# Performance work log

Measured on AMD Instinct MI355X. Metric: run time of the kernel, lower is better.

Reference implementation:

```python
import jax, jax.numpy as jnp
import numpy as np

B, S, D = 4, 4096, 256  # batch, seq_len, input_dims == num_hiddens
NEG = -1e9

def setup_inputs() -> dict:
    key = jax.random.key(0)
    ks = jax.random.split(key, 9)
    sd = 1.0 / np.sqrt(D)
    x = jax.random.normal(ks[0], (B, S, D), dtype=jnp.float32)
    mask = jnp.tril(jnp.ones((S, S), dtype=jnp.int32))[None, :, :]  # [1,S,S] causal
    # Linear params: y = x @ W.T + b (torch convention); store as [in,out] for einsum
    wq = jax.random.uniform(ks[1], (D, D), jnp.float32, -sd, sd)
    bq = jax.random.uniform(ks[2], (D,), jnp.float32, -sd, sd)
    wk = jax.random.uniform(ks[3], (D, D), jnp.float32, -sd, sd)
    bk = jax.random.uniform(ks[4], (D,), jnp.float32, -sd, sd)
    wv = jax.random.uniform(ks[5], (D, D), jnp.float32, -sd, sd)
    bv = jax.random.uniform(ks[6], (D,), jnp.float32, -sd, sd)
    wo = jax.random.uniform(ks[7], (D, D), jnp.float32, -sd, sd)
    bo = jax.random.uniform(ks[8], (D,), jnp.float32, -sd, sd)
    return {"x": x, "mask": mask, "wq": wq, "bq": bq, "wk": wk, "bk": bk,
            "wv": wv, "bv": bv, "wo": wo, "bo": bo}

def reference(x, mask, wq, bq, wk, bk, wv, bv, wo, bo):
    # Single-head scaled dot-product self-attention (dropout = identity / eval mode)
    q = jnp.einsum('bsd,df->bsf', x, wq) + bq
    k = jnp.einsum('bsd,df->bsf', x, wk) + bk
    v = jnp.einsum('bsd,df->bsf', x, wv) + bv
    attn = jnp.einsum('bqf,bkf->bqk', q, k) / jnp.sqrt(jnp.float32(q.shape[-1]))
    attn = jnp.where(mask == 0, NEG, attn)  # masked_fill(mask==0, -1e9)
    attn = jax.nn.softmax(attn, axis=-1)
    score = jnp.einsum('bqk,bkf->bqf', attn, v)
    out = jnp.einsum('bsf,fd->bsd', score, wo) + bo
    return out
```

## Files before the change

kernel.cpp:

```cpp
#include <hip/hip_runtime.h>
#include <stdint.h>
#include <type_traits>

typedef __attribute__((ext_vector_type(8))) short short8;
typedef __attribute__((ext_vector_type(4))) short s16x4;
typedef __attribute__((ext_vector_type(4))) float f32x4;

#define S_LEN 4096
#define D_DIM 256
#define BATCH 4

__device__ __forceinline__ f32x4 mfma16(short8 a, short8 b, f32x4 c) {
    return __builtin_amdgcn_mfma_f32_16x16x32_bf16(a, b, c, 0, 0, 0);
}

__device__ __forceinline__ short f2bf(float x) {
    uint32_t u = __float_as_uint(x);
    uint32_t r = (u + 0x7FFFu + ((u >> 16) & 1u)) >> 16;
    return (short)r;
}
__device__ __forceinline__ float bf2f(short s) {
    uint32_t u = ((uint32_t)(uint16_t)s) << 16;
    return __uint_as_float(u);
}

__device__ __forceinline__ void gload16(const short* g, short* l) {
    __builtin_amdgcn_global_load_lds(
        (const __attribute__((address_space(1))) void*)g,
        (__attribute__((address_space(3))) void*)l, 16, 0, 0);
}

__global__ __launch_bounds__(256) void xbf_conv(
    const float* __restrict__ x, short* __restrict__ xb)
{
    int i = blockIdx.x * 256 + threadIdx.x;
    f32x4 a = *reinterpret_cast<const f32x4*>(x + (size_t)i * 8);
    f32x4 b = *reinterpret_cast<const f32x4*>(x + (size_t)i * 8 + 4);
    short8 r;
#pragma unroll
    for (int k = 0; k < 4; ++k) r[k] = f2bf(a[k]);
#pragma unroll
    for (int k = 0; k < 4; ++k) r[k + 4] = f2bf(b[k]);
    *reinterpret_cast<short8*>(xb + (size_t)i * 8) = r;
}

__global__ __launch_bounds__(256) void transpose_w(
    const float* __restrict__ wq, const float* __restrict__ wk,
    const float* __restrict__ wv, const float* __restrict__ wo,
    short* __restrict__ out)
{
    __shared__ float t[16][17];
    const float* in = blockIdx.z == 0 ? wq : blockIdx.z == 1 ? wk
                    : blockIdx.z == 2 ? wv : wo;
    short* o = out + (size_t)blockIdx.z * 65536;
    const int x0 = blockIdx.x * 16, y0 = blockIdx.y * 16;
    const int tx = threadIdx.x, ty = threadIdx.y;
    t[ty][tx] = in[(y0 + ty) * 256 + x0 + tx];
    __syncthreads();
    o[(size_t)(x0 + ty) * 256 + y0 + tx] = f2bf(t[tx][ty]);
}

__global__ __launch_bounds__(256) void gemm_qkv(
    const short* __restrict__ A, const short* __restrict__ Bt,
    const float* __restrict__ bq, const float* __restrict__ bk,
    const float* __restrict__ bv,
    short* __restrict__ QF, short* __restrict__ KF, short* __restrict__ VF)
{
    __shared__ short As[128 * 64];
    __shared__ short Bs[128 * 64];
    const int tid = threadIdx.x;
    const int lane = tid & 63;
    const int w = tid >> 6;
    const int wr = w >> 1, wc = w & 1;
    const int lo = lane & 15, hi = lane >> 4;
    const size_t m0 = (size_t)blockIdx.y * 128, n0 = (size_t)blockIdx.x * 128;
    const int reg = (int)(n0 >> 8);
    const float* bias = reg == 0 ? bq : (reg == 1 ? bk : bv);

    f32x4 acc[4][4] = {};

    for (int kt = 0; kt < 4; ++kt) {
#pragma unroll
        for (int i = 0; i < 4; ++i) {
            int c = i * 4 + w;
            int s = c * 64 + lane;
            int row = s >> 3, ke = (s & 7) * 8;
            gload16(A  + (m0 + row) * 256 + kt * 64 + ke, As + c * 512);
            gload16(Bt + (n0 + row) * 256 + kt * 64 + ke, Bs + c * 512);
        }
        __syncthreads();
#pragma unroll
        for (int kk = 0; kk < 2; ++kk) {
            short8 af[4], bf[4];
#pragma unroll
            for (int m = 0; m < 4; ++m)
                af[m] = *reinterpret_cast<const short8*>(&As[(wr * 64 + m * 16 + lo) * 64 + kk * 32 + hi * 8]);
#pragma unroll
            for (int n = 0; n < 4; ++n)
                bf[n] = *reinterpret_cast<const short8*>(&Bs[(wc * 64 + n * 16 + lo) * 64 + kk * 32 + hi * 8]);
#pragma unroll
            for (int m = 0; m < 4; ++m)
#pragma unroll
                for (int n = 0; n < 4; ++n)
                    acc[m][n] = mfma16(af[m], bf[n], acc[m][n]);
        }
        __syncthreads();
    }

#pragma unroll
    for (int m = 0; m < 4; ++m) {
#pragma unroll
        for (int n = 0; n < 4; ++n) {
#pragma unroll
            for (int j = 0; j < 4; ++j) {
                size_t row = m0 + wr * 64 + m * 16 + hi * 4 + j;
                int f = (int)((n0 + wc * 64 + n * 16 + lo) & 255);
                float v = acc[m][n][j] + bias[f];
                int b = (int)(row >> 12), R = (int)(row & 4095);
                if (reg == 0) {
                    int jt = R >> 4, lk = R & 15;
                    int kk = f >> 5, q = f & 31, hk = q >> 3, e = q & 7;
                    QF[((((size_t)(b * 256 + jt) * 8 + kk) * 64) + hk * 16 + lk) * 8 + e] = f2bf(v);
                } else if (reg == 1) {
                    int ktile = R >> 6, nn = (R >> 4) & 3, lk = R & 15;
                    int kk = f >> 5, q = f & 31, hk = q >> 3, e = q & 7;
                    KF[(((((size_t)(b * 64 + ktile) * 8 + kk) * 4 + nn) * 64) + hk * 16 + lk) * 8 + e] = f2bf(v);
                } else {
                    int ktile = R >> 6, t6 = R & 63, k2 = t6 >> 5, r5 = t6 & 31;
                    int hk = r5 >> 3, e = r5 & 7;
                    int nf = f >> 4, lk = f & 15;
                    VF[(((((size_t)(b * 64 + ktile) * 2 + k2) * 16 + nf) * 64) + hk * 16 + lk) * 8 + e] = f2bf(v);
                }
            }
        }
    }
}

__global__ __launch_bounds__(256) void gemm_out(
    const short* __restrict__ A, const short* __restrict__ Bt,
    const float* __restrict__ bias, float* __restrict__ C, int ldc)
{
    __shared__ short As[128 * 64];
    __shared__ short Bs[128 * 64];
    const int tid = threadIdx.x;
    const int lane = tid & 63;
    const int w = tid >> 6;
    const int wr = w >> 1, wc = w & 1;
    const int lo = lane & 15, hi = lane >> 4;
    const size_t m0 = (size_t)blockIdx.y * 128, n0 = (size_t)blockIdx.x * 128;

    f32x4 acc[4][4] = {};

    for (int kt = 0; kt < 4; ++kt) {
#pragma unroll
        for (int i = 0; i < 4; ++i) {
            int c = i * 4 + w;
            int s = c * 64 + lane;
            int row = s >> 3, ke = (s & 7) * 8;
            gload16(A  + (m0 + row) * 256 + kt * 64 + ke, As + c * 512);
            gload16(Bt + (n0 + row) * 256 + kt * 64 + ke, Bs + c * 512);
        }
        __syncthreads();
#pragma unroll
        for (int kk = 0; kk < 2; ++kk) {
            short8 af[4], bf[4];
#pragma unroll
            for (int m = 0; m < 4; ++m)
                af[m] = *reinterpret_cast<const short8*>(&As[(wr * 64 + m * 16 + lo) * 64 + kk * 32 + hi * 8]);
#pragma unroll
            for (int n = 0; n < 4; ++n)
                bf[n] = *reinterpret_cast<const short8*>(&Bs[(wc * 64 + n * 16 + lo) * 64 + kk * 32 + hi * 8]);
#pragma unroll
            for (int m = 0; m < 4; ++m)
#pragma unroll
                for (int n = 0; n < 4; ++n)
                    acc[m][n] = mfma16(af[m], bf[n], acc[m][n]);
        }
        __syncthreads();
    }

#pragma unroll
    for (int m = 0; m < 4; ++m)
#pragma unroll
        for (int n = 0; n < 4; ++n)
#pragma unroll
            for (int j = 0; j < 4; ++j) {
                size_t row = m0 + wr * 64 + m * 16 + hi * 4 + j;
                size_t col = n0 + wc * 64 + n * 16 + lo;
                C[row * (size_t)ldc + col] = acc[m][n][j] + bias[col];
            }
}

template <int NSPLIT, bool DIRECT>
__global__ __launch_bounds__(512) void attn_fwd(
    const short* __restrict__ Qf, const short* __restrict__ Kf,
    const short* __restrict__ Vf, short* __restrict__ PO,
    float* __restrict__ PML, short* __restrict__ Sc)
{
    __shared__ short Ks[2][64 * 256];
    __shared__ short Vs[2][64 * 256];
    __shared__ short P[8][16 * 64];

    const int tid = threadIdx.x;
    const int lane = tid & 63;
    const int w = tid >> 6;
    const int lo = lane & 15, hi = lane >> 4;
    const int bx = (int)blockIdx.x;
    const int m = bx / (BATCH * NSPLIT);
    const int r = bx % (BATCH * NSPLIT);
    const int b = r % BATCH;
    const int p = r / BATCH;

    auto stage = [&](int buf, int kt) {
        const short* Kt = Kf + (size_t)(b * 64 + kt) * 16384;
        const short* Vt = Vf + (size_t)(b * 64 + kt) * 16384;
#pragma unroll
        for (int c4 = 0; c4 < 4; ++c4) {
            int c = c4 * 8 + w;
            gload16(Kt + c * 512 + lane * 8, &Ks[buf][c * 512]);
            gload16(Vt + c * 512 + lane * 8, &Vs[buf][c * 512]);
        }
    };

    for (int half = 0; half < 2; ++half) {
        const int j = half == 0 ? (31 - m) : m;
        const int q0 = j * 128;
        const int last = 2 * j + 1;

        short8 qv[8];
#pragma unroll
        for (int kk = 0; kk < 8; ++kk)
            qv[kk] = *reinterpret_cast<const short8*>(
                Qf + (((size_t)(b * 256 + j * 8 + w) * 8 + kk) * 64 + lane) * 8);

        f32x4 o[16] = {};
        float mrow[4] = {-1e30f, -1e30f, -1e30f, -1e30f};
        float lrow[4] = {0.f, 0.f, 0.f, 0.f};

        int cur = 0;
        if (p <= last) stage(0, p);
        __syncthreads();

        for (int kt = p; kt <= last; kt += NSPLIT) {
            if (kt + NSPLIT <= last) stage(cur ^ 1, kt + NSPLIT);

            f32x4 s4[4] = {};
            __builtin_amdgcn_s_setprio(1);
#pragma unroll
            for (int kk = 0; kk < 8; ++kk) {
#pragma unroll
                for (int n = 0; n < 4; ++n) {
                    short8 kf = *reinterpret_cast<const short8*>(&Ks[cur][((kk * 4 + n) * 64 + lane) * 8]);
                    s4[n] = mfma16(qv[kk], kf, s4[n]);
                }
            }
            __builtin_amdgcn_s_setprio(0);

            const bool diag = (kt >= 2 * j);
            float pm[4] = {-1e30f, -1e30f, -1e30f, -1e30f};
#pragma unroll
            for (int n = 0; n < 4; ++n) {
#pragma unroll
                for (int jj = 0; jj < 4; ++jj) {
                    float v = s4[n][jj] * 0.0625f;
                    if (diag) {
                        int rl = q0 + w * 16 + hi * 4 + jj;
                        int cl = kt * 64 + n * 16 + lo;
                        if (cl > rl) v = -1e30f;
                    }
                    s4[n][jj] = v;
                    pm[jj] = fmaxf(pm[jj], v);
                }
            }
#pragma unroll
            for (int off = 1; off < 16; off <<= 1)
#pragma unroll
                for (int jj = 0; jj < 4; ++jj)
                    pm[jj] = fmaxf(pm[jj], __shfl_xor(pm[jj], off));

            float sc[4], lsum[4];
#pragma unroll
            for (int jj = 0; jj < 4; ++jj) {
                float mn = fmaxf(mrow[jj], pm[jj]);
                sc[jj] = __expf(mrow[jj] - mn);
                mrow[jj] = mn;
                lsum[jj] = 0.f;
            }
#pragma unroll
            for (int n = 0; n < 4; ++n)
#pragma unroll
                for (int jj = 0; jj < 4; ++jj) {
                    float pv = __expf(s4[n][jj] - mrow[jj]);
                    s4[n][jj] = pv;
                    lsum[jj] += pv;
                }
#pragma unroll
            for (int off = 1; off < 16; off <<= 1)
#pragma unroll
                for (int jj = 0; jj < 4; ++jj)
                    lsum[jj] += __shfl_xor(lsum[jj], off);
#pragma unroll
            for (int jj = 0; jj < 4; ++jj)
                lrow[jj] = lrow[jj] * sc[jj] + lsum[jj];
#pragma unroll
            for (int nf = 0; nf < 16; ++nf)
#pragma unroll
                for (int jj = 0; jj < 4; ++jj)
                    o[nf][jj] *= sc[jj];

#pragma unroll
            for (int n = 0; n < 4; ++n)
#pragma unroll
                for (int jj = 0; jj < 4; ++jj) {
                    int row16 = hi * 4 + jj;
                    int idx = (row16 * 64 + (n * 16 + lo)) ^ ((row16 & 7) << 3);
                    P[w][idx] = f2bf(s4[n][jj]);
                }

            __builtin_amdgcn_s_setprio(1);
#pragma unroll
            for (int k2 = 0; k2 < 2; ++k2) {
                short8 pa = *reinterpret_cast<const short8*>(
                    &P[w][(lo * 64 + k2 * 32 + hi * 8) ^ ((lo & 7) << 3)]);
#pragma unroll
                for (int nf = 0; nf < 16; ++nf) {
                    short8 vf = *reinterpret_cast<const short8*>(&Vs[cur][((k2 * 16 + nf) * 64 + lane) * 8]);
                    o[nf] = mfma16(pa, vf, o[nf]);
                }
            }
            __builtin_amdgcn_s_setprio(0);
            __syncthreads();
            cur ^= 1;
        }

        if constexpr (DIRECT) {
            short* Sb = Sc + (size_t)b * S_LEN * D_DIM;
#pragma unroll
            for (int nf = 0; nf < 16; ++nf)
#pragma unroll
                for (int jj = 0; jj < 4; ++jj) {
                    size_t row = q0 + w * 16 + hi * 4 + jj;
                    Sb[row * D_DIM + nf * 16 + lo] = f2bf(o[nf][jj] / lrow[jj]);
                }
        } else {
            size_t pb = (size_t)(b * 32 + j) * NSPLIT + p;
            short* POb = PO + pb * (128 * 256);
            float* PMLb = PML + pb * 256;
#pragma unroll
            for (int nf = 0; nf < 16; ++nf)
#pragma unroll
                for (int jj = 0; jj < 4; ++jj)
                    POb[(w * 16 + hi * 4 + jj) * 256 + nf * 16 + lo] = f2bf(o[nf][jj]);
            if (lo == 0)
#pragma unroll
                for (int jj = 0; jj < 4; ++jj) {
                    PMLb[w * 16 + hi * 4 + jj] = mrow[jj];
                    PMLb[128 + w * 16 + hi * 4 + jj] = lrow[jj];
                }
        }
    }
}

template <int NSPLIT>
__global__ __launch_bounds__(256) void attn_merge(
    const short* __restrict__ PO, const float* __restrict__ PML,
    short* __restrict__ Sc)
{
    const int bid = (int)blockIdx.x;
    const int b = bid >> 6, s6 = bid & 63;
    const int j = s6 >> 1, h = s6 & 1;
    const int t = threadIdx.x;
    const int lr = t >> 2;
    const int c0 = (t & 3) << 6;
    const int row128 = h * 64 + lr;

    float mm[NSPLIT], ll[NSPLIT], e[NSPLIT];
    float M = -3.3e38f;
#pragma unroll
    for (int p = 0; p < NSPLIT; ++p) {
        size_t pb = (size_t)(b * 32 + j) * NSPLIT + p;
        mm[p] = PML[pb * 256 + row128];
        ll[p] = PML[pb * 256 + 128 + row128];
        M = fmaxf(M, mm[p]);
    }
    float L = 0.f;
#pragma unroll
    for (int p = 0; p < NSPLIT; ++p) { e[p] = __expf(mm[p] - M); L += ll[p] * e[p]; }
    const float inv = 1.0f / L;

    short* Sb = Sc + (size_t)b * S_LEN * D_DIM + (size_t)(j * 128 + row128) * D_DIM;
#pragma unroll
    for (int k = 0; k < 8; ++k) {
        float acc[8] = {};
#pragma unroll
        for (int p = 0; p < NSPLIT; ++p) {
            size_t pb = (size_t)(b * 32 + j) * NSPLIT + p;
            short8 v = *reinterpret_cast<const short8*>(
                &PO[pb * 32768 + (size_t)row128 * 256 + c0 + k * 8]);
#pragma unroll
            for (int ii = 0; ii < 8; ++ii) acc[ii] += bf2f(v[ii]) * e[p];
        }
        short8 sv;
#pragma unroll
        for (int ii = 0; ii < 8; ++ii) sv[ii] = f2bf(acc[ii] * inv);
        *reinterpret_cast<short8*>(&Sb[c0 + k * 8]) = sv;
    }
}

extern "C" void kernel_launch(void* const* d_in, const int* in_sizes, int n_in,
                              void* d_out, int out_size, void* d_ws, size_t ws_size,
                              hipStream_t stream)
{
    const float* x  = (const float*)d_in[0];
    const float* wq = (const float*)d_in[2];
    const float* bq = (const float*)d_in[3];
    const float* wk = (const float*)d_in[4];
    const float* bk = (const float*)d_in[5];
    const float* wv = (const float*)d_in[6];
    const float* bv = (const float*)d_in[7];
    const float* wo = (const float*)d_in[8];
    const float* bo = (const float*)d_in[9];
    float* out = (float*)d_out;

    const size_t NTOK = (size_t)BATCH * S_LEN;
    const size_t TD = NTOK * D_DIM;
    short* WT = (short*)d_ws;
    short* QF = WT + 4 * 65536;
    short* KF = QF + TD;
    short* VF = KF + TD;
    short* xb = VF + TD;
    short* POs = xb;
    short* Sw = QF;
    const size_t po_off_b = (size_t)(4 * 65536 + 3 * TD) * 2;
    const size_t part_b = TD * 2 + (size_t)128 * 256 * 4;
    const size_t xb_end_b = po_off_b + TD * 2;

    const int M = (int)NTOK;

    xbf_conv<<<dim3(2048), 256, 0, stream>>>(x, xb);
    transpose_w<<<dim3(16, 16, 4), dim3(16, 16), 0, stream>>>(wq, wk, wv, wo, WT);
    gemm_qkv<<<dim3(6, M / 128), 256, 0, stream>>>(xb, WT, bq, bk, bv, QF, KF, VF);

    if (ws_size >= po_off_b + 4 * part_b && ws_size >= xb_end_b) {
        float* PML = (float*)(POs + 4 * TD);
        attn_fwd<4, false><<<dim3(16 * BATCH * 4), 512, 0, stream>>>(QF, KF, VF, POs, PML, Sw);
        attn_merge<4><<<dim3(256), 256, 0, stream>>>(POs, PML, Sw);
    } else if (ws_size >= po_off_b + 2 * part_b && ws_size >= xb_end_b) {
        float* PML = (float*)(POs + 2 * TD);
        attn_fwd<2, false><<<dim3(16 * BATCH * 2), 512, 0, stream>>>(QF, KF, VF, POs, PML, Sw);
        attn_merge<2><<<dim3(256), 256, 0, stream>>>(POs, PML, Sw);
    } else {
        attn_fwd<1, true><<<dim3(16 * BATCH), 512, 0, stream>>>(QF, KF, VF, nullptr, nullptr, Sw);
    }

    gemm_out<<<dim3(2, M / 128), 256, 0, stream>>>(Sw, WT + 3 * 65536, bo, out, 256);
}
```

Before: 136.6 us.

## Fuse split-KV merge into output projection GEMM with precomputed scale factors

Removes the separate attention merge kernel. A tiny kernel now turns each partial's per-row max and sum into a single combined scale factor, stored in place. The output GEMM then builds its A tile on the fly by scaling and summing the NSPLIT bf16 partial outputs. This avoids writing and re-reading the merged score tensor. In exchange, each of the two column blocks redoes the merge reads, and a kernel launch is added.

```diff
diff --git a/kernel.cpp b/kernel.cpp
--- a/kernel.cpp
+++ b/kernel.cpp
@@ -191,6 +191,109 @@
             }
 }
 
+template <int NSPLIT>
+__global__ __launch_bounds__(128) void calc_sfac(float* __restrict__ PML)
+{
+    const int bid = (int)blockIdx.x;
+    const int lr = threadIdx.x;
+    const size_t base = (size_t)bid * NSPLIT;
+
+    float mm[NSPLIT], ll[NSPLIT];
+    float M = -3.3e38f;
+#pragma unroll
+    for (int p = 0; p < NSPLIT; ++p) {
+        mm[p] = PML[(base + p) * 256 + lr];
+        ll[p] = PML[(base + p) * 256 + 128 + lr];
+        M = fmaxf(M, mm[p]);
+    }
+    float L = 0.f, e[NSPLIT];
+#pragma unroll
+    for (int p = 0; p < NSPLIT; ++p) { e[p] = __expf(mm[p] - M); L += ll[p] * e[p]; }
+    const float inv = 1.0f / L;
+#pragma unroll
+    for (int p = 0; p < NSPLIT; ++p)
+        PML[(base + p) * 256 + lr] = e[p] * inv;
+}
+
+template <int NSPLIT>
+__global__ __launch_bounds__(256) void gemm_out_fused(
+    const short* __restrict__ PO, const float* __restrict__ PML,
+    const short* __restrict__ Bt, const float* __restrict__ bias,
+    float* __restrict__ C)
+{
+    __shared__ short As[128 * 64];
+    __shared__ short Bs[128 * 64];
+    const int tid = threadIdx.x;
+    const int lane = tid & 63;
+    const int w = tid >> 6;
+    const int wr = w >> 1, wc = w & 1;
+    const int lo = lane & 15, hi = lane >> 4;
+    const size_t m0 = (size_t)blockIdx.y * 128, n0 = (size_t)blockIdx.x * 128;
+
+    f32x4 acc[4][4] = {};
+
+    for (int kt = 0; kt < 4; ++kt) {
+        short8 va[4];
+#pragma unroll
+        for (int i = 0; i < 4; ++i) {
+            int c = i * 4 + w;
+            int s = c * 64 + lane;
+            int row = s >> 3, ke = (s & 7) * 8;
+            size_t grow = m0 + row;
+            int b = (int)(grow >> 12), R = (int)(grow & 4095);
+            int jq = R >> 7, lr = R & 127;
+            size_t pb0 = (size_t)(b * 32 + jq) * NSPLIT;
+
+            float a8[8] = {};
+#pragma unroll
+            for (int p = 0; p < NSPLIT; ++p) {
+                float sf = PML[(pb0 + p) * 256 + lr];
+                short8 v = *reinterpret_cast<const short8*>(
+                    &PO[(pb0 + p) * 32768 + (size_t)lr * 256 + kt * 64 + ke]);
+#pragma unroll
+                for (int ii = 0; ii < 8; ++ii) a8[ii] += bf2f(v[ii]) * sf;
+            }
+#pragma unroll
+            for (int ii = 0; ii < 8; ++ii) va[i][ii] = f2bf(a8[ii]);
+
+            gload16(Bt + (n0 + row) * 256 + kt * 64 + ke, Bs + c * 512);
+        }
+#pragma unroll
+        for (int i = 0; i < 4; ++i) {
+            int c = i * 4 + w;
+            *reinterpret_cast<short8*>(&As[(c * 64 + lane) * 8]) = va[i];
+        }
+        __syncthreads();
+#pragma unroll
+        for (int kk = 0; kk < 2; ++kk) {
+            short8 af[4], bf[4];
+#pragma unroll
+            for (int m = 0; m < 4; ++m)
+                af[m] = *reinterpret_cast<const short8*>(&As[(wr * 64 + m * 16 + lo) * 64 + kk * 32 + hi * 8]);
+#pragma unroll
+            for (int n = 0; n < 4; ++n)
+                bf[n] = *reinterpret_cast<const short8*>(&Bs[(wc * 64 + n * 16 + lo) * 64 + kk * 32 + hi * 8]);
+#pragma unroll
+            for (int m = 0; m < 4; ++m)
+#pragma unroll
+                for (int n = 0; n < 4; ++n)
+                    acc[m][n] = mfma16(af[m], bf[n], acc[m][n]);
+        }
+        __syncthreads();
+    }
+
+#pragma unroll
+    for (int m = 0; m < 4; ++m)
+#pragma unroll
+        for (int n = 0; n < 4; ++n)
+#pragma unroll
+            for (int j = 0; j < 4; ++j) {
+                size_t row = m0 + wr * 64 + m * 16 + hi * 4 + j;
+                size_t col = n0 + wc * 64 + n * 16 + lo;
+                C[row * (size_t)256 + col] = acc[m][n][j] + bias[col];
+            }
+}
+
 template <int NSPLIT, bool DIRECT>
 __global__ __launch_bounds__(512) void attn_fwd(
     const short* __restrict__ Qf, const short* __restrict__ Kf,
@@ -358,52 +461,6 @@
                     PMLb[128 + w * 16 + hi * 4 + jj] = lrow[jj];
                 }
         }
-    }
-}
-
-template <int NSPLIT>
-__global__ __launch_bounds__(256) void attn_merge(
-    const short* __restrict__ PO, const float* __restrict__ PML,
-    short* __restrict__ Sc)
-{
-    const int bid = (int)blockIdx.x;
-    const int b = bid >> 6, s6 = bid & 63;
-    const int j = s6 >> 1, h = s6 & 1;
-    const int t = threadIdx.x;
-    const int lr = t >> 2;
-    const int c0 = (t & 3) << 6;
-    const int row128 = h * 64 + lr;
-
-    float mm[NSPLIT], ll[NSPLIT], e[NSPLIT];
-    float M = -3.3e38f;
-#pragma unroll
-    for (int p = 0; p < NSPLIT; ++p) {
-        size_t pb = (size_t)(b * 32 + j) * NSPLIT + p;
-        mm[p] = PML[pb * 256 + row128];
-        ll[p] = PML[pb * 256 + 128 + row128];
-        M = fmaxf(M, mm[p]);
-    }
-    float L = 0.f;
-#pragma unroll
-    for (int p = 0; p < NSPLIT; ++p) { e[p] = __expf(mm[p] - M); L += ll[p] * e[p]; }
-    const float inv = 1.0f / L;
-
-    short* Sb = Sc + (size_t)b * S_LEN * D_DIM + (size_t)(j * 128 + row128) * D_DIM;
-#pragma unroll
-    for (int k = 0; k < 8; ++k) {
-        float acc[8] = {};
-#pragma unroll
-        for (int p = 0; p < NSPLIT; ++p) {
-            size_t pb = (size_t)(b * 32 + j) * NSPLIT + p;
-            short8 v = *reinterpret_cast<const short8*>(
-                &PO[pb * 32768 + (size_t)row128 * 256 + c0 + k * 8]);
-#pragma unroll
-            for (int ii = 0; ii < 8; ++ii) acc[ii] += bf2f(v[ii]) * e[p];
-        }
-        short8 sv;
-#pragma unroll
-        for (int ii = 0; ii < 8; ++ii) sv[ii] = f2bf(acc[ii] * inv);
-        *reinterpret_cast<short8*>(&Sb[c0 + k * 8]) = sv;
     }
 }
 
@@ -444,14 +501,15 @@
     if (ws_size >= po_off_b + 4 * part_b && ws_size >= xb_end_b) {
         float* PML = (float*)(POs + 4 * TD);
         attn_fwd<4, false><<<dim3(16 * BATCH * 4), 512, 0, stream>>>(QF, KF, VF, POs, PML, Sw);
-        attn_merge<4><<<dim3(256), 256, 0, stream>>>(POs, PML, Sw);
+        calc_sfac<4><<<dim3(128), 128, 0, stream>>>(PML);
+        gemm_out_fused<4><<<dim3(2, M / 128), 256, 0, stream>>>(POs, PML, WT + 3 * 65536, bo, out);
     } else if (ws_size >= po_off_b + 2 * part_b && ws_size >= xb_end_b) {
         float* PML = (float*)(POs + 2 * TD);
         attn_fwd<2, false><<<dim3(16 * BATCH * 2), 512, 0, stream>>>(QF, KF, VF, POs, PML, Sw);
-        attn_merge<2><<<dim3(256), 256, 0, stream>>>(POs, PML, Sw);
+        calc_sfac<2><<<dim3(128), 128, 0, stream>>>(PML);
+        gemm_out_fused<2><<<dim3(2, M / 128), 256, 0, stream>>>(POs, PML, WT + 3 * 65536, bo, out);
     } else {
         attn_fwd<1, true><<<dim3(16 * BATCH), 512, 0, stream>>>(QF, KF, VF, nullptr, nullptr, Sw);
-    }
-
-    gemm_out<<<dim3(2, M / 128), 256, 0, stream>>>(Sw, WT + 3 * 65536, bo, out, 256);
-}
+        gemm_out<<<dim3(2, M / 128), 256, 0, stream>>>(Sw, WT + 3 * 65536, bo, out, 256);
+    }
+}
```

Measured after the change: 120.2 us (median of 2 runs). 12.0% less time.
